# Performance work log

Measured on AMD Instinct MI355X. Metric: run time of the kernel, lower is better.

## Reference

```python
import jax, jax.numpy as jnp
import numpy as np

B, C, L = 8, 64, 65536  # batch, channels, flattened H*W
GN_EPS = 1e-5


def setup_inputs() -> dict:
    key = jax.random.key(0)
    ks = jax.random.split(key, 8)
    return {
        "x": jax.random.normal(ks[0], (B, C, L), dtype=jnp.float32),
        "inj0": jax.random.normal(ks[1], (B, C, L), dtype=jnp.float32),
        "inj1": jax.random.normal(ks[2], (B, C, L), dtype=jnp.float32),
        "residual": jax.random.normal(ks[3], (B, C, L), dtype=jnp.float32),
        "gate_w": jax.random.normal(ks[4], (C, C), dtype=jnp.float32) * (1.0 / np.sqrt(C)),
        "gate_b": jax.random.normal(ks[5], (C,), dtype=jnp.float32) * 0.01,
        "fuse_w": jax.random.normal(ks[6], (C, C), dtype=jnp.float32) * (1.0 / np.sqrt(C)),
        "fuse_b": jax.random.normal(ks[7], (C,), dtype=jnp.float32) * 0.01,
        "gn_w": jnp.ones((C,), dtype=jnp.float32),
        "gn_b": jnp.zeros((C,), dtype=jnp.float32),
    }


def _conv1x1(w, b, t):
    # Conv1d with kernel_size=1: [O,C] x [B,C,L] -> [B,O,L]
    return jnp.einsum('oc,bcl->bol', w, t) + b[None, :, None]


def reference(x, inj0, inj1, residual, gate_w, gate_b, fuse_w, fuse_b, gn_w, gn_b):
    # per-injection gate + elementwise multiply, summed over injections
    acc = jnp.zeros_like(x)
    for inj in (inj0, inj1):  # fixed small list of injection features
        acc = acc + x * _conv1x1(gate_w, gate_b, inj + x)
    # fuse conv + residual + ReLU (dropout p=0 -> identity)
    out = jax.nn.relu(_conv1x1(fuse_w, fuse_b, acc) + residual)
    # GroupNorm(num_groups=1): normalize over (C, L) per sample, per-channel affine
    mean = jnp.mean(out, axis=(1, 2), keepdims=True)
    var = jnp.var(out, axis=(1, 2), keepdims=True)
    out = (out - mean) * jax.lax.rsqrt(var + GN_EPS)
    return out * gn_w[None, :, None] + gn_b[None, :, None]
```

## Files before the change

### kernel.cpp

```cpp
#include <hip/hip_runtime.h>
#include <stdint.h>

#define Bv 8
#define Cv 64
#define Lv 65536
#define TPB 512
#define COLS 256
#define BLKS_PER_B (Lv / COLS)
#define GRID1 (Bv * BLKS_PER_B)


typedef __attribute__((ext_vector_type(8))) short short8;
typedef __attribute__((ext_vector_type(4))) float f32x4;

#define SSTRIDE 260

__device__ __forceinline__ uint16_t f2bf(float f) {
    uint32_t u = __float_as_uint(f);
    uint32_t r = u + 0x7FFFu + ((u >> 16) & 1u);
    return (uint16_t)(r >> 16);
}
__device__ __forceinline__ uint32_t pack2bf(float lo, float hi) {
    return (uint32_t)f2bf(lo) | ((uint32_t)f2bf(hi) << 16);
}

__global__ void pass1(const float* __restrict__ x, const float* __restrict__ inj0,
                      const float* __restrict__ inj1, const float* __restrict__ resid,
                      const float* __restrict__ gate_w, const float* __restrict__ gate_b,
                      const float* __restrict__ fuse_w, const float* __restrict__ fuse_b,
                      float* __restrict__ out, float* __restrict__ partials)
{
    __shared__ uint32_t s_buf[16 * SSTRIDE];
    __shared__ uint32_t w_lds[2][64][36];
    __shared__ float cinit[2][64];
    __shared__ float r1[TPB], r2[TPB];

    const int tid  = threadIdx.x;
    const int lane = tid & 63;
    const int w    = tid >> 6;
    const int g    = lane >> 4;
    const int ln   = lane & 15;

    const int b    = blockIdx.x >> 8;
    const int lb   = blockIdx.x & 255;
    const int col0 = lb * COLS;
    const int bCL  = b * (Cv * Lv);

    {
        const int mat = tid >> 8;
        const int m   = (tid >> 2) & 63;
        const int k0  = (tid & 3) << 4;
        const float* wsrc = mat ? fuse_w : gate_w;
        const float4* w4 = reinterpret_cast<const float4*>(wsrc + m * 64 + k0);
        uint32_t* dst = &w_lds[mat][m][k0 >> 1];
        #pragma unroll
        for (int q = 0; q < 4; ++q) {
            const float4 v = w4[q];
            dst[2 * q]     = pack2bf(v.x, v.y);
            dst[2 * q + 1] = pack2bf(v.z, v.w);
        }
        if (tid < 64) {
            cinit[0][tid] = 2.0f * gate_b[tid];
            cinit[1][tid] = fuse_b[tid];
        }
    }
    __syncthreads();

    f32x4 D1[4][2];
    #pragma unroll
    for (int oc = 0; oc < 4; ++oc) {
        const float4 cb = *reinterpret_cast<const float4*>(&cinit[0][16 * oc + 4 * g]);
        D1[oc][0][0] = cb.x; D1[oc][0][1] = cb.y;
        D1[oc][0][2] = cb.z; D1[oc][0][3] = cb.w;
        D1[oc][1] = D1[oc][0];
    }

    #pragma unroll 1
    for (int kh = 0; kh < 2; ++kh) {
        #pragma unroll
        for (int uu = 0; uu < 2; ++uu) {
            const int u  = tid + uu * TPB;
            const int kp = u >> 6;
            const int c  = (u & 63) << 2;
            const int rA = bCL + (32 * kh + 2 * kp) * Lv + col0 + c;
            const int rB = rA + Lv;
            const float4 xA = *reinterpret_cast<const float4*>(x    + rA);
            const float4 aA = *reinterpret_cast<const float4*>(inj0 + rA);
            const float4 bA = *reinterpret_cast<const float4*>(inj1 + rA);
            const float4 xB = *reinterpret_cast<const float4*>(x    + rB);
            const float4 aB = *reinterpret_cast<const float4*>(inj0 + rB);
            const float4 bB = *reinterpret_cast<const float4*>(inj1 + rB);
            uint4 dw;
            dw.x = pack2bf(aA.x + bA.x + 2.0f * xA.x, aB.x + bB.x + 2.0f * xB.x);
            dw.y = pack2bf(aA.y + bA.y + 2.0f * xA.y, aB.y + bB.y + 2.0f * xB.y);
            dw.z = pack2bf(aA.z + bA.z + 2.0f * xA.z, aB.z + bB.z + 2.0f * xB.z);
            dw.w = pack2bf(aA.w + bA.w + 2.0f * xA.w, aB.w + bB.w + 2.0f * xB.w);
            *reinterpret_cast<uint4*>(&s_buf[kp * SSTRIDE + c]) = dw;
        }
        __syncthreads();

        #pragma unroll
        for (int nt = 0; nt < 2; ++nt) {
            const int n = ln + 16 * (2 * w + nt);
            uint4 Bf;
            Bf.x = s_buf[(4 * g + 0) * SSTRIDE + n];
            Bf.y = s_buf[(4 * g + 1) * SSTRIDE + n];
            Bf.z = s_buf[(4 * g + 2) * SSTRIDE + n];
            Bf.w = s_buf[(4 * g + 3) * SSTRIDE + n];
            #pragma unroll
            for (int oc = 0; oc < 4; ++oc) {
                const int m = ln + 16 * oc;
                const uint4 A = *reinterpret_cast<const uint4*>(&w_lds[0][m][16 * kh + 4 * g]);
                D1[oc][nt] = __builtin_amdgcn_mfma_f32_16x16x32_bf16(
                    __builtin_bit_cast(short8, A), __builtin_bit_cast(short8, Bf),
                    D1[oc][nt], 0, 0, 0);
            }
        }
        __syncthreads();
    }

    f32x4 D2[4][2];
    #pragma unroll
    for (int oc = 0; oc < 4; ++oc) {
        const float4 cb = *reinterpret_cast<const float4*>(&cinit[1][16 * oc + 4 * g]);
        D2[oc][0][0] = cb.x; D2[oc][0][1] = cb.y;
        D2[oc][0][2] = cb.z; D2[oc][0][3] = cb.w;
        D2[oc][1] = D2[oc][0];
    }
    #pragma unroll
    for (int kh = 0; kh < 2; ++kh) {
        #pragma unroll
        for (int nt = 0; nt < 2; ++nt) {
            const int n  = ln + 16 * (2 * w + nt);
            const int cg = bCL + col0 + n;
            #pragma unroll
            for (int oc2 = 0; oc2 < 2; ++oc2) {
                const int oc = 2 * kh + oc2;
                const int m0 = 16 * oc + 4 * g;
                float av[4];
                #pragma unroll
                for (int j = 0; j < 4; ++j)
                    av[j] = x[cg + (m0 + j) * Lv] * D1[oc][nt][j];
                s_buf[(8 * oc2 + 2 * g) * SSTRIDE + n]     = pack2bf(av[0], av[1]);
                s_buf[(8 * oc2 + 2 * g + 1) * SSTRIDE + n] = pack2bf(av[2], av[3]);
            }
        }
        __syncthreads();
        #pragma unroll
        for (int nt = 0; nt < 2; ++nt) {
            const int n = ln + 16 * (2 * w + nt);
            uint4 Bf;
            Bf.x = s_buf[(4 * g + 0) * SSTRIDE + n];
            Bf.y = s_buf[(4 * g + 1) * SSTRIDE + n];
            Bf.z = s_buf[(4 * g + 2) * SSTRIDE + n];
            Bf.w = s_buf[(4 * g + 3) * SSTRIDE + n];
            #pragma unroll
            for (int oc = 0; oc < 4; ++oc) {
                const int m = ln + 16 * oc;
                const uint4 A = *reinterpret_cast<const uint4*>(&w_lds[1][m][16 * kh + 4 * g]);
                D2[oc][nt] = __builtin_amdgcn_mfma_f32_16x16x32_bf16(
                    __builtin_bit_cast(short8, A), __builtin_bit_cast(short8, Bf),
                    D2[oc][nt], 0, 0, 0);
            }
        }
        __syncthreads();
    }

    float lsum = 0.0f, lsq = 0.0f;
    {
        float* uf = reinterpret_cast<float*>(s_buf);
        const int rowin = tid >> 5;
        const int cl    = tid & 31;
        #pragma unroll
        for (int ck = 0; ck < 4; ++ck) {
            #pragma unroll
            for (int nt = 0; nt < 2; ++nt) {
                const int n = ln + 16 * (2 * w + nt);
                #pragma unroll
                for (int j = 0; j < 4; ++j)
                    uf[(4 * g + j) * SSTRIDE + n] = D2[ck][nt][j];
            }
            const int m   = 16 * ck + rowin;
            const int gbm = bCL + m * Lv + col0;
            const float4 ra = *reinterpret_cast<const float4*>(&resid[gbm + 4 * cl]);
            const float4 rb = *reinterpret_cast<const float4*>(&resid[gbm + 4 * cl + 128]);
            __syncthreads();
            float4 va = *reinterpret_cast<const float4*>(&uf[rowin * SSTRIDE + 4 * cl]);
            float4 vb = *reinterpret_cast<const float4*>(&uf[rowin * SSTRIDE + 4 * cl + 128]);
            va.x = fmaxf(va.x + ra.x, 0.0f); va.y = fmaxf(va.y + ra.y, 0.0f);
            va.z = fmaxf(va.z + ra.z, 0.0f); va.w = fmaxf(va.w + ra.w, 0.0f);
            vb.x = fmaxf(vb.x + rb.x, 0.0f); vb.y = fmaxf(vb.y + rb.y, 0.0f);
            vb.z = fmaxf(vb.z + rb.z, 0.0f); vb.w = fmaxf(vb.w + rb.w, 0.0f);
            *reinterpret_cast<float4*>(&out[gbm + 4 * cl])       = va;
            *reinterpret_cast<float4*>(&out[gbm + 4 * cl + 128]) = vb;
            lsum += (va.x + va.y) + (va.z + va.w) + (vb.x + vb.y) + (vb.z + vb.w);
            lsq = fmaf(va.x, va.x, lsq); lsq = fmaf(va.y, va.y, lsq);
            lsq = fmaf(va.z, va.z, lsq); lsq = fmaf(va.w, va.w, lsq);
            lsq = fmaf(vb.x, vb.x, lsq); lsq = fmaf(vb.y, vb.y, lsq);
            lsq = fmaf(vb.z, vb.z, lsq); lsq = fmaf(vb.w, vb.w, lsq);
            __syncthreads();
        }
    }

    r1[tid] = lsum; r2[tid] = lsq;
    __syncthreads();
    #pragma unroll
    for (int st = TPB / 2; st > 0; st >>= 1) {
        if (tid < st) { r1[tid] += r1[tid + st]; r2[tid] += r2[tid + st]; }
        __syncthreads();
    }
    if (tid == 0) {
        partials[2 * blockIdx.x]     = r1[0];
        partials[2 * blockIdx.x + 1] = r2[0];
    }
}

__global__ __launch_bounds__(256)
void pass2(const float* __restrict__ partials, const float* __restrict__ gn_w,
           const float* __restrict__ gn_b, float* __restrict__ sb)
{
    __shared__ float r1[256], r2[256];
    __shared__ float mean_s, rs_s;
    const int b = blockIdx.x, tid = threadIdx.x;
    r1[tid] = partials[2 * (b * 256 + tid)];
    r2[tid] = partials[2 * (b * 256 + tid) + 1];
    __syncthreads();
    #pragma unroll
    for (int st = 128; st > 0; st >>= 1) {
        if (tid < st) { r1[tid] += r1[tid + st]; r2[tid] += r2[tid + st]; }
        __syncthreads();
    }
    if (tid == 0) {
        const float n = (float)Cv * (float)Lv;
        const float mean = r1[0] / n;
        const float var  = r2[0] / n - mean * mean;
        mean_s = mean;
        rs_s   = rsqrtf(var + 1e-5f);
    }
    __syncthreads();
    if (tid < Cv) {
        const float sc = gn_w[tid] * rs_s;
        sb[b * Cv + tid]           = sc;
        sb[Bv * Cv + b * Cv + tid] = fmaf(-mean_s, sc, gn_b[tid]);
    }
}

__global__ __launch_bounds__(256)
void pass3(float* __restrict__ out, const float* __restrict__ sb)
{
    const int total4 = (Bv * Cv * Lv) / 4;
    for (int i = blockIdx.x * blockDim.x + threadIdx.x; i < total4;
         i += gridDim.x * blockDim.x) {
        const int row = i >> 14;
        const float sc = sb[row];
        const float bi = sb[Bv * Cv + row];
        float4 v = reinterpret_cast<float4*>(out)[i];
        v.x = fmaf(v.x, sc, bi);
        v.y = fmaf(v.y, sc, bi);
        v.z = fmaf(v.z, sc, bi);
        v.w = fmaf(v.w, sc, bi);
        reinterpret_cast<float4*>(out)[i] = v;
    }
}

extern "C" void kernel_launch(void* const* d_in, const int* in_sizes, int n_in,
                              void* d_out, int out_size, void* d_ws, size_t ws_size,
                              hipStream_t stream)
{
    const float* x      = (const float*)d_in[0];
    const float* inj0   = (const float*)d_in[1];
    const float* inj1   = (const float*)d_in[2];
    const float* resid  = (const float*)d_in[3];
    const float* gate_w = (const float*)d_in[4];
    const float* gate_b = (const float*)d_in[5];
    const float* fuse_w = (const float*)d_in[6];
    const float* fuse_b = (const float*)d_in[7];
    const float* gn_w   = (const float*)d_in[8];
    const float* gn_b   = (const float*)d_in[9];

    float* out      = (float*)d_out;
    float* ws       = (float*)d_ws;
    float* partials = ws;
    float* sb       = ws + 2 * GRID1;

    hipLaunchKernelGGL(pass1, dim3(GRID1), dim3(TPB), 0, stream,
                       x, inj0, inj1, resid, gate_w, gate_b, fuse_w, fuse_b,
                       out, partials);
    hipLaunchKernelGGL(pass2, dim3(Bv), dim3(256), 0, stream,
                       partials, gn_w, gn_b, sb);
    hipLaunchKernelGGL(pass3, dim3(2048), dim3(256), 0, stream, out, sb);
}
```

Before: 186.6 us.

## Stage x in LDS as bf16 and use wave-shuffle block reduction

The x tile is packed to bf16 and kept in a new LDS buffer while the gate input is built, so the gating multiply reads it from LDS instead of reloading x from global memory with strided per-channel loads. The end-of-block sum/sum-of-squares reduction now uses wave shuffles and a small per-wave LDS array, replacing the shared-memory tree that needed many barriers. In exchange, LDS use per block grows, which may lower occupancy, and x in the gating multiply is rounded to bf16, a small loss of precision.

```diff
diff --git a/kernel.cpp b/kernel.cpp
--- a/kernel.cpp
+++ b/kernel.cpp
@@ -23,6 +23,8 @@
 __device__ __forceinline__ uint32_t pack2bf(float lo, float hi) {
     return (uint32_t)f2bf(lo) | ((uint32_t)f2bf(hi) << 16);
 }
+__device__ __forceinline__ float bf_lo(uint32_t u) { return __uint_as_float(u << 16); }
+__device__ __forceinline__ float bf_hi(uint32_t u) { return __uint_as_float(u & 0xFFFF0000u); }
 
 __global__ void pass1(const float* __restrict__ x, const float* __restrict__ inj0,
                       const float* __restrict__ inj1, const float* __restrict__ resid,
@@ -31,9 +33,10 @@
                       float* __restrict__ out, float* __restrict__ partials)
 {
     __shared__ uint32_t s_buf[16 * SSTRIDE];
+    __shared__ uint32_t x_lds[2][16 * SSTRIDE];
     __shared__ uint32_t w_lds[2][64][36];
     __shared__ float cinit[2][64];
-    __shared__ float r1[TPB], r2[TPB];
+    __shared__ float wred[16];
 
     const int tid  = threadIdx.x;
     const int lane = tid & 63;
@@ -96,6 +99,12 @@
             dw.z = pack2bf(aA.z + bA.z + 2.0f * xA.z, aB.z + bB.z + 2.0f * xB.z);
             dw.w = pack2bf(aA.w + bA.w + 2.0f * xA.w, aB.w + bB.w + 2.0f * xB.w);
             *reinterpret_cast<uint4*>(&s_buf[kp * SSTRIDE + c]) = dw;
+            uint4 dx;
+            dx.x = pack2bf(xA.x, xB.x);
+            dx.y = pack2bf(xA.y, xB.y);
+            dx.z = pack2bf(xA.z, xB.z);
+            dx.w = pack2bf(xA.w, xB.w);
+            *reinterpret_cast<uint4*>(&x_lds[kh][kp * SSTRIDE + c]) = dx;
         }
         __syncthreads();
 
@@ -127,22 +136,24 @@
         D2[oc][0][2] = cb.z; D2[oc][0][3] = cb.w;
         D2[oc][1] = D2[oc][0];
     }
-    #pragma unroll
+    #pragma unroll 1
     for (int kh = 0; kh < 2; ++kh) {
         #pragma unroll
         for (int nt = 0; nt < 2; ++nt) {
-            const int n  = ln + 16 * (2 * w + nt);
-            const int cg = bCL + col0 + n;
+            const int n = ln + 16 * (2 * w + nt);
             #pragma unroll
             for (int oc2 = 0; oc2 < 2; ++oc2) {
                 const int oc = 2 * kh + oc2;
-                const int m0 = 16 * oc + 4 * g;
+                const int kpA = 8 * oc2 + 2 * g;
+                const uint32_t u0 = x_lds[kh][kpA * SSTRIDE + n];
+                const uint32_t u1 = x_lds[kh][(kpA + 1) * SSTRIDE + n];
                 float av[4];
-                #pragma unroll
-                for (int j = 0; j < 4; ++j)
-                    av[j] = x[cg + (m0 + j) * Lv] * D1[oc][nt][j];
-                s_buf[(8 * oc2 + 2 * g) * SSTRIDE + n]     = pack2bf(av[0], av[1]);
-                s_buf[(8 * oc2 + 2 * g + 1) * SSTRIDE + n] = pack2bf(av[2], av[3]);
+                av[0] = bf_lo(u0) * D1[oc][nt][0];
+                av[1] = bf_hi(u0) * D1[oc][nt][1];
+                av[2] = bf_lo(u1) * D1[oc][nt][2];
+                av[3] = bf_hi(u1) * D1[oc][nt][3];
+                s_buf[kpA * SSTRIDE + n]       = pack2bf(av[0], av[1]);
+                s_buf[(kpA + 1) * SSTRIDE + n] = pack2bf(av[2], av[3]);
             }
         }
         __syncthreads();
@@ -202,16 +213,19 @@
         }
     }
 
-    r1[tid] = lsum; r2[tid] = lsq;
+    #pragma unroll
+    for (int st = 1; st < 64; st <<= 1) {
+        lsum += __shfl_xor(lsum, st);
+        lsq  += __shfl_xor(lsq,  st);
+    }
+    if (lane == 0) { wred[2 * w] = lsum; wred[2 * w + 1] = lsq; }
     __syncthreads();
-    #pragma unroll
-    for (int st = TPB / 2; st > 0; st >>= 1) {
-        if (tid < st) { r1[tid] += r1[tid + st]; r2[tid] += r2[tid + st]; }
-        __syncthreads();
-    }
     if (tid == 0) {
-        partials[2 * blockIdx.x]     = r1[0];
-        partials[2 * blockIdx.x + 1] = r2[0];
+        float s = 0.0f, q = 0.0f;
+        #pragma unroll
+        for (int i = 0; i < 8; ++i) { s += wred[2 * i]; q += wred[2 * i + 1]; }
+        partials[2 * blockIdx.x]     = s;
+        partials[2 * blockIdx.x + 1] = q;
     }
 }
 
```

Result: slower. 245.6 us (+31.6%).

## Load all input channels up front, interleave gate and fuse GEMMs per phase, shuffle-reduce stats

Applied to the files above, without the earlier changes.

The kernel now loads and packs the full 64-channel gate input into a doubled LDS buffer in one go. It then runs two phases, each computing half of the gate-conv output channels over the full K and immediately feeding them into the fuse GEMM through a separate LDS buffer. This cuts the number of block-wide barriers and lets all global loads issue together. The final sum and sum-of-squares reduction switches from a shared-memory tree to wavefront shuffles plus a small cross-wave sum. The cost is more LDS per block, which may lower occupancy, and more loads held in flight at once.

```diff
diff --git a/kernel.cpp b/kernel.cpp
--- a/kernel.cpp
+++ b/kernel.cpp
@@ -30,10 +30,11 @@
                       const float* __restrict__ fuse_w, const float* __restrict__ fuse_b,
                       float* __restrict__ out, float* __restrict__ partials)
 {
-    __shared__ uint32_t s_buf[16 * SSTRIDE];
+    __shared__ uint32_t s_buf[32 * SSTRIDE];
+    __shared__ uint32_t a_buf[16 * SSTRIDE];
     __shared__ uint32_t w_lds[2][64][36];
     __shared__ float cinit[2][64];
-    __shared__ float r1[TPB], r2[TPB];
+    __shared__ float wred[16];
 
     const int tid  = threadIdx.x;
     const int lane = tid & 63;
@@ -64,60 +65,28 @@
             cinit[1][tid] = fuse_b[tid];
         }
     }
+
+    #pragma unroll
+    for (int uu = 0; uu < 4; ++uu) {
+        const int u  = tid + uu * TPB;
+        const int kp = u >> 6;
+        const int c  = (u & 63) << 2;
+        const int rA = bCL + (2 * kp) * Lv + col0 + c;
+        const int rB = rA + Lv;
+        const float4 xA = *reinterpret_cast<const float4*>(x    + rA);
+        const float4 aA = *reinterpret_cast<const float4*>(inj0 + rA);
+        const float4 bA = *reinterpret_cast<const float4*>(inj1 + rA);
+        const float4 xB = *reinterpret_cast<const float4*>(x    + rB);
+        const float4 aB = *reinterpret_cast<const float4*>(inj0 + rB);
+        const float4 bB = *reinterpret_cast<const float4*>(inj1 + rB);
+        uint4 dw;
+        dw.x = pack2bf(aA.x + bA.x + 2.0f * xA.x, aB.x + bB.x + 2.0f * xB.x);
+        dw.y = pack2bf(aA.y + bA.y + 2.0f * xA.y, aB.y + bB.y + 2.0f * xB.y);
+        dw.z = pack2bf(aA.z + bA.z + 2.0f * xA.z, aB.z + bB.z + 2.0f * xB.z);
+        dw.w = pack2bf(aA.w + bA.w + 2.0f * xA.w, aB.w + bB.w + 2.0f * xB.w);
+        *reinterpret_cast<uint4*>(&s_buf[kp * SSTRIDE + c]) = dw;
+    }
     __syncthreads();
-
-    f32x4 D1[4][2];
-    #pragma unroll
-    for (int oc = 0; oc < 4; ++oc) {
-        const float4 cb = *reinterpret_cast<const float4*>(&cinit[0][16 * oc + 4 * g]);
-        D1[oc][0][0] = cb.x; D1[oc][0][1] = cb.y;
-        D1[oc][0][2] = cb.z; D1[oc][0][3] = cb.w;
-        D1[oc][1] = D1[oc][0];
-    }
-
-    #pragma unroll 1
-    for (int kh = 0; kh < 2; ++kh) {
-        #pragma unroll
-        for (int uu = 0; uu < 2; ++uu) {
-            const int u  = tid + uu * TPB;
-            const int kp = u >> 6;
-            const int c  = (u & 63) << 2;
-            const int rA = bCL + (32 * kh + 2 * kp) * Lv + col0 + c;
-            const int rB = rA + Lv;
-            const float4 xA = *reinterpret_cast<const float4*>(x    + rA);
-            const float4 aA = *reinterpret_cast<const float4*>(inj0 + rA);
-            const float4 bA = *reinterpret_cast<const float4*>(inj1 + rA);
-            const float4 xB = *reinterpret_cast<const float4*>(x    + rB);
-            const float4 aB = *reinterpret_cast<const float4*>(inj0 + rB);
-            const float4 bB = *reinterpret_cast<const float4*>(inj1 + rB);
-            uint4 dw;
-            dw.x = pack2bf(aA.x + bA.x + 2.0f * xA.x, aB.x + bB.x + 2.0f * xB.x);
-            dw.y = pack2bf(aA.y + bA.y + 2.0f * xA.y, aB.y + bB.y + 2.0f * xB.y);
-            dw.z = pack2bf(aA.z + bA.z + 2.0f * xA.z, aB.z + bB.z + 2.0f * xB.z);
-            dw.w = pack2bf(aA.w + bA.w + 2.0f * xA.w, aB.w + bB.w + 2.0f * xB.w);
-            *reinterpret_cast<uint4*>(&s_buf[kp * SSTRIDE + c]) = dw;
-        }
-        __syncthreads();
-
-        #pragma unroll
-        for (int nt = 0; nt < 2; ++nt) {
-            const int n = ln + 16 * (2 * w + nt);
-            uint4 Bf;
-            Bf.x = s_buf[(4 * g + 0) * SSTRIDE + n];
-            Bf.y = s_buf[(4 * g + 1) * SSTRIDE + n];
-            Bf.z = s_buf[(4 * g + 2) * SSTRIDE + n];
-            Bf.w = s_buf[(4 * g + 3) * SSTRIDE + n];
-            #pragma unroll
-            for (int oc = 0; oc < 4; ++oc) {
-                const int m = ln + 16 * oc;
-                const uint4 A = *reinterpret_cast<const uint4*>(&w_lds[0][m][16 * kh + 4 * g]);
-                D1[oc][nt] = __builtin_amdgcn_mfma_f32_16x16x32_bf16(
-                    __builtin_bit_cast(short8, A), __builtin_bit_cast(short8, Bf),
-                    D1[oc][nt], 0, 0, 0);
-            }
-        }
-        __syncthreads();
-    }
 
     f32x4 D2[4][2];
     #pragma unroll
@@ -127,37 +96,76 @@
         D2[oc][0][2] = cb.z; D2[oc][0][3] = cb.w;
         D2[oc][1] = D2[oc][0];
     }
-    #pragma unroll
-    for (int kh = 0; kh < 2; ++kh) {
+
+    float lsum = 0.0f, lsq = 0.0f;
+
+    #pragma unroll 1
+    for (int ph = 0; ph < 2; ++ph) {
+        f32x4 D1[2][2];
+        #pragma unroll
+        for (int o2 = 0; o2 < 2; ++o2) {
+            const int oc = 2 * ph + o2;
+            const float4 cb = *reinterpret_cast<const float4*>(&cinit[0][16 * oc + 4 * g]);
+            D1[o2][0][0] = cb.x; D1[o2][0][1] = cb.y;
+            D1[o2][0][2] = cb.z; D1[o2][0][3] = cb.w;
+            D1[o2][1] = D1[o2][0];
+        }
+        #pragma unroll
+        for (int nt = 0; nt < 2; ++nt) {
+            const int n = ln + 16 * (2 * w + nt);
+            uint4 B0, B1;
+            B0.x = s_buf[(4 * g + 0) * SSTRIDE + n];
+            B0.y = s_buf[(4 * g + 1) * SSTRIDE + n];
+            B0.z = s_buf[(4 * g + 2) * SSTRIDE + n];
+            B0.w = s_buf[(4 * g + 3) * SSTRIDE + n];
+            B1.x = s_buf[(16 + 4 * g + 0) * SSTRIDE + n];
+            B1.y = s_buf[(16 + 4 * g + 1) * SSTRIDE + n];
+            B1.z = s_buf[(16 + 4 * g + 2) * SSTRIDE + n];
+            B1.w = s_buf[(16 + 4 * g + 3) * SSTRIDE + n];
+            #pragma unroll
+            for (int o2 = 0; o2 < 2; ++o2) {
+                const int m = ln + 16 * (2 * ph + o2);
+                const uint4 A0 = *reinterpret_cast<const uint4*>(&w_lds[0][m][4 * g]);
+                const uint4 A1 = *reinterpret_cast<const uint4*>(&w_lds[0][m][16 + 4 * g]);
+                D1[o2][nt] = __builtin_amdgcn_mfma_f32_16x16x32_bf16(
+                    __builtin_bit_cast(short8, A0), __builtin_bit_cast(short8, B0),
+                    D1[o2][nt], 0, 0, 0);
+                D1[o2][nt] = __builtin_amdgcn_mfma_f32_16x16x32_bf16(
+                    __builtin_bit_cast(short8, A1), __builtin_bit_cast(short8, B1),
+                    D1[o2][nt], 0, 0, 0);
+            }
+        }
+
         #pragma unroll
         for (int nt = 0; nt < 2; ++nt) {
             const int n  = ln + 16 * (2 * w + nt);
             const int cg = bCL + col0 + n;
             #pragma unroll
-            for (int oc2 = 0; oc2 < 2; ++oc2) {
-                const int oc = 2 * kh + oc2;
-                const int m0 = 16 * oc + 4 * g;
+            for (int o2 = 0; o2 < 2; ++o2) {
+                const int m0 = 16 * (2 * ph + o2) + 4 * g;
                 float av[4];
                 #pragma unroll
                 for (int j = 0; j < 4; ++j)
-                    av[j] = x[cg + (m0 + j) * Lv] * D1[oc][nt][j];
-                s_buf[(8 * oc2 + 2 * g) * SSTRIDE + n]     = pack2bf(av[0], av[1]);
-                s_buf[(8 * oc2 + 2 * g + 1) * SSTRIDE + n] = pack2bf(av[2], av[3]);
+                    av[j] = x[cg + (m0 + j) * Lv] * D1[o2][nt][j];
+                const int kpA = 8 * o2 + 2 * g;
+                a_buf[kpA * SSTRIDE + n]       = pack2bf(av[0], av[1]);
+                a_buf[(kpA + 1) * SSTRIDE + n] = pack2bf(av[2], av[3]);
             }
         }
         __syncthreads();
+
         #pragma unroll
         for (int nt = 0; nt < 2; ++nt) {
             const int n = ln + 16 * (2 * w + nt);
             uint4 Bf;
-            Bf.x = s_buf[(4 * g + 0) * SSTRIDE + n];
-            Bf.y = s_buf[(4 * g + 1) * SSTRIDE + n];
-            Bf.z = s_buf[(4 * g + 2) * SSTRIDE + n];
-            Bf.w = s_buf[(4 * g + 3) * SSTRIDE + n];
+            Bf.x = a_buf[(4 * g + 0) * SSTRIDE + n];
+            Bf.y = a_buf[(4 * g + 1) * SSTRIDE + n];
+            Bf.z = a_buf[(4 * g + 2) * SSTRIDE + n];
+            Bf.w = a_buf[(4 * g + 3) * SSTRIDE + n];
             #pragma unroll
             for (int oc = 0; oc < 4; ++oc) {
                 const int m = ln + 16 * oc;
-                const uint4 A = *reinterpret_cast<const uint4*>(&w_lds[1][m][16 * kh + 4 * g]);
+                const uint4 A = *reinterpret_cast<const uint4*>(&w_lds[1][m][16 * ph + 4 * g]);
                 D2[oc][nt] = __builtin_amdgcn_mfma_f32_16x16x32_bf16(
                     __builtin_bit_cast(short8, A), __builtin_bit_cast(short8, Bf),
                     D2[oc][nt], 0, 0, 0);
@@ -166,9 +174,8 @@
         __syncthreads();
     }
 
-    float lsum = 0.0f, lsq = 0.0f;
     {
-        float* uf = reinterpret_cast<float*>(s_buf);
+        float* uf = reinterpret_cast<float*>(a_buf);
         const int rowin = tid >> 5;
         const int cl    = tid & 31;
         #pragma unroll
@@ -202,16 +209,19 @@
         }
     }
 
-    r1[tid] = lsum; r2[tid] = lsq;
+    #pragma unroll
+    for (int st = 1; st < 64; st <<= 1) {
+        lsum += __shfl_xor(lsum, st);
+        lsq  += __shfl_xor(lsq,  st);
+    }
+    if (lane == 0) { wred[2 * w] = lsum; wred[2 * w + 1] = lsq; }
     __syncthreads();
-    #pragma unroll
-    for (int st = TPB / 2; st > 0; st >>= 1) {
-        if (tid < st) { r1[tid] += r1[tid + st]; r2[tid] += r2[tid + st]; }
-        __syncthreads();
-    }
     if (tid == 0) {
-        partials[2 * blockIdx.x]     = r1[0];
-        partials[2 * blockIdx.x + 1] = r2[0];
+        float s = 0.0f, q = 0.0f;
+        #pragma unroll
+        for (int i = 0; i < 8; ++i) { s += wred[2 * i]; q += wred[2 * i + 1]; }
+        partials[2 * blockIdx.x]     = s;
+        partials[2 * blockIdx.x + 1] = q;
     }
 }
 
```

New measurement: 187.5 us. Within noise of the previous version (+0.5%).
